# Kernel optimization log

Hardware: AMD Instinct MI355X
Metric: run time of the kernel (lower is better)

The kernel has to match this reference:

```python
import jax, jax.numpy as jnp
import numpy as np

TOP_K = 2
NORM_TOPK = True


def setup_inputs() -> dict:
    key = jax.random.key(0)
    k1, k2, k3, k4 = jax.random.split(key, 4)
    B, S, H = 2, 1024, 2048
    E, I = 16, 768
    hidden_states = jax.random.normal(k1, (B, S, H), dtype=jnp.float32)
    gate_w = jax.random.normal(k2, (E, H), dtype=jnp.float32) * 0.02
    gate_up_w = jax.random.normal(k3, (E, 2 * I, H), dtype=jnp.float32) * 0.02
    down_w = jax.random.normal(k4, (E, H, I), dtype=jnp.float32) * 0.02
    return {
        "hidden_states": hidden_states,
        "gate_w": gate_w,
        "gate_up_w": gate_up_w,
        "down_w": down_w,
        "top_k": TOP_K,
    }


def reference(hidden_states, gate_w, gate_up_w, down_w, top_k):
    B, S, H = hidden_states.shape
    E = gate_w.shape[0]
    x = hidden_states.reshape(-1, H)  # [T, H]
    T = x.shape[0]

    # Router: softmax in float32 (as in torch F.softmax(..., dtype=torch.float))
    router_logits = x @ gate_w.T  # [T, E]
    probs = jax.nn.softmax(router_logits.astype(jnp.float32), axis=-1)
    top_w, top_idx = jax.lax.top_k(probs, top_k)  # [T, k]
    if NORM_TOPK:
        top_w = top_w / jnp.sum(top_w, axis=-1, keepdims=True)
    top_w = top_w.astype(x.dtype)

    # Dense combine weights [T, E]: routing weight where selected, 0 elsewhere.
    comb = jnp.sum(jax.nn.one_hot(top_idx, E, dtype=x.dtype) * top_w[..., None], axis=1)

    # SwiGLU expert MLPs evaluated for all experts, combined with sparse weights.
    gu = jnp.einsum("th,efh->tef", x, gate_up_w)  # [T, E, 2I]
    g, u = jnp.split(gu, 2, axis=-1)
    h = jax.nn.silu(g) * u  # [T, E, I]
    y = jnp.einsum("tei,ehi->teh", h, down_w)  # [T, E, H]
    out = jnp.einsum("teh,te->th", y, comb)  # [T, H]

    return out.reshape(B, S, H), router_logits
```

## Files before the change

### kernel.cpp

```cpp
#include <hip/hip_runtime.h>
#include <hip/hip_bf16.h>
#include <stdint.h>

#define T_TOK 2048
#define H_DIM 2048
#define E_NUM 16
#define I_DIM 768

typedef __bf16 bf16;
typedef __bf16 bf16x4 __attribute__((ext_vector_type(4)));
typedef __bf16 bf16x8 __attribute__((ext_vector_type(8)));
typedef float f32x4 __attribute__((ext_vector_type(4)));

__device__ __forceinline__ void async_cp16(void* l, const void* g) {
    __builtin_amdgcn_global_load_lds(
        (const __attribute__((address_space(1))) void*)g,
        (__attribute__((address_space(3))) void*)l, 16, 0, 0);
}

__global__ __launch_bounds__(256) void router_kernel(
    const float* __restrict__ x, const float* __restrict__ gw,
    float* __restrict__ logits, int* __restrict__ cnt,
    int* __restrict__ tok_list, float* __restrict__ wgt_list,
    bf16* __restrict__ xb)
{
    const int t = blockIdx.x;
    const int tid = threadIdx.x;
    const int lane = tid & 63, wid = tid >> 6;

    double part[E_NUM];
#pragma unroll
    for (int e = 0; e < E_NUM; ++e) part[e] = 0.0;

#pragma unroll
    for (int it = 0; it < 2; ++it) {
        int h = it * 1024 + tid * 4;
        float4 xv = *(const float4*)(x + (size_t)t * H_DIM + h);
        bf16x4 xb4 = { (bf16)xv.x, (bf16)xv.y, (bf16)xv.z, (bf16)xv.w };
        *(bf16x4*)(xb + (size_t)t * H_DIM + h) = xb4;
#pragma unroll
        for (int e = 0; e < E_NUM; ++e) {
            float4 wv = *(const float4*)(gw + (size_t)e * H_DIM + h);
            part[e] += (double)xv.x * (double)wv.x + (double)xv.y * (double)wv.y
                     + (double)xv.z * (double)wv.z + (double)xv.w * (double)wv.w;
        }
    }
#pragma unroll
    for (int off = 32; off > 0; off >>= 1)
#pragma unroll
        for (int e = 0; e < E_NUM; ++e)
            part[e] += __shfl_down(part[e], off);

    __shared__ double sh[4][E_NUM];
    __shared__ float lg[E_NUM];
    if (lane == 0)
#pragma unroll
        for (int e = 0; e < E_NUM; ++e) sh[wid][e] = part[e];
    __syncthreads();
    if (tid < E_NUM) {
        float v = (float)(sh[0][tid] + sh[1][tid] + sh[2][tid] + sh[3][tid]);
        lg[tid] = v;
        logits[(size_t)t * E_NUM + tid] = v;
    }
    __syncthreads();
    if (tid == 0) {
        int i0 = 0; float v0 = lg[0];
#pragma unroll
        for (int e = 1; e < E_NUM; ++e) if (lg[e] > v0) { v0 = lg[e]; i0 = e; }
        int i1 = -1; float v1 = -3.4e38f;
#pragma unroll
        for (int e = 0; e < E_NUM; ++e) if (e != i0 && lg[e] > v1) { v1 = lg[e]; i1 = e; }
        float w0 = 1.0f / (1.0f + __expf(v1 - v0));
        float w1 = 1.0f - w0;
        int p0 = atomicAdd(&cnt[i0], 1);
        tok_list[i0 * T_TOK + p0] = t; wgt_list[i0 * T_TOK + p0] = w0;
        int p1 = atomicAdd(&cnt[i1], 1);
        tok_list[i1 * T_TOK + p1] = t; wgt_list[i1 * T_TOK + p1] = w1;
    }
}

__global__ void scan_kernel(const int* __restrict__ cnt, int* __restrict__ offs)
{
    if (threadIdx.x == 0) {
        int o = 0;
        for (int e = 0; e < E_NUM; ++e) { offs[e] = o; o += cnt[e]; }
    }
}

__global__ __launch_bounds__(256, 2) void gateup_kernel(
    const bf16* __restrict__ xb, const float* __restrict__ gup,
    const int* __restrict__ cnt, const int* __restrict__ offs,
    const int* __restrict__ tok_list, bf16* __restrict__ hbuf)
{
    const int e = blockIdx.z;
    const int count = cnt[e];
    const int row0 = blockIdx.y * 64;
    if (row0 >= count) return;
    const int i0 = blockIdx.x * 64;
    const int hoff = offs[e];
    const int tid = threadIdx.x;
    const int lane = tid & 63, wid = tid >> 6;

    __shared__ __align__(16) bf16 As[2][64 * 64];
    __shared__ __align__(16) float Bs[2][128 * 64];

    int raA0 = tid >> 3, sA0 = tid & 7;
    int raA1 = raA0 + 32;
    int cA0 = sA0 ^ (raA0 & 7);
    int cA1 = sA0 ^ (raA1 & 7);
    int tr0 = row0 + raA0; if (tr0 >= count) tr0 = count - 1;
    int tr1 = row0 + raA1; if (tr1 >= count) tr1 = count - 1;
    const bf16* srcA0 = xb + (size_t)tok_list[e * T_TOK + tr0] * H_DIM + cA0 * 8;
    const bf16* srcA1 = xb + (size_t)tok_list[e * T_TOK + tr1] * H_DIM + cA1 * 8;
    const int dA0 = (wid * 64) * 8;
    const int dA1 = (wid * 64 + 256) * 8;

    const float* srcB[8]; int dB[8];
#pragma unroll
    for (int i = 0; i < 8; ++i) {
        int idx = i * 256 + tid;
        int r = idx >> 4, s = idx & 15;
        int c = s ^ (r & 15);
        int is_u = (r >> 5) & 1;
        int ioff = (r >> 6) * 32 + (r & 31);
        size_t grow = (size_t)e * (2 * I_DIM) + (size_t)is_u * I_DIM + i0 + ioff;
        srcB[i] = gup + grow * H_DIM + c * 4;
        dB[i] = (i * 256 + wid * 64) * 4;
    }

    f32x4 acc[2][4];
#pragma unroll
    for (int a = 0; a < 2; ++a)
#pragma unroll
        for (int b = 0; b < 4; ++b) acc[a][b] = (f32x4){0.f, 0.f, 0.f, 0.f};

    const int la = lane & 15, lq = lane >> 4;
    const int wm = wid >> 1, wn = wid & 1;

    auto stage = [&](int buf, int k0) {
        async_cp16(&As[buf][dA0], srcA0 + k0);
        async_cp16(&As[buf][dA1], srcA1 + k0);
#pragma unroll
        for (int i = 0; i < 8; ++i) async_cp16(&Bs[buf][dB[i]], srcB[i] + k0);
    };

    stage(0, 0);
    __syncthreads();
    int cur = 0;
    for (int k0 = 0; k0 < H_DIM; k0 += 64) {
        if (k0 + 64 < H_DIM) stage(cur ^ 1, k0 + 64);
        const bf16* Asc = As[cur];
        const float* Bsc = Bs[cur];
#pragma unroll
        for (int ks = 0; ks < 2; ++ks) {
            bf16x8 af[2], bfr[4];
            int chA = ks * 4 + lq;
            int c0 = ks * 8 + lq * 2;
#pragma unroll
            for (int mt = 0; mt < 2; ++mt) {
                int row = 32 * wm + 16 * mt + la;
                int sl = chA ^ (row & 7);
                af[mt] = *(const bf16x8*)(Asc + (size_t)(row * 8 + sl) * 8);
            }
#pragma unroll
            for (int nt = 0; nt < 4; ++nt) {
                int row = 64 * wn + 16 * nt + la;
                int s0 = c0 ^ (row & 15);
                int s1 = s0 ^ 1;
                f32x4 v0 = *(const f32x4*)(Bsc + (size_t)(row * 16 + s0) * 4);
                f32x4 v1 = *(const f32x4*)(Bsc + (size_t)(row * 16 + s1) * 4);
                bfr[nt] = (bf16x8){ (bf16)v0.x, (bf16)v0.y, (bf16)v0.z, (bf16)v0.w,
                                    (bf16)v1.x, (bf16)v1.y, (bf16)v1.z, (bf16)v1.w };
            }
#pragma unroll
            for (int mt = 0; mt < 2; ++mt)
#pragma unroll
                for (int nt = 0; nt < 4; ++nt)
                    acc[mt][nt] = __builtin_amdgcn_mfma_f32_16x16x32_bf16(af[mt], bfr[nt], acc[mt][nt], 0, 0, 0);
        }
        __syncthreads();
        cur ^= 1;
    }

#pragma unroll
    for (int mt = 0; mt < 2; ++mt)
#pragma unroll
        for (int p = 0; p < 2; ++p)
#pragma unroll
            for (int r = 0; r < 4; ++r) {
                int trow = 32 * wm + 16 * mt + lq * 4 + r;
                if (row0 + trow < count) {
                    float g = acc[mt][p][r], u = acc[mt][p + 2][r];
                    float hv = (g / (1.0f + __expf(-g))) * u;
                    int col = i0 + 32 * wn + 16 * p + la;
                    hbuf[(size_t)(hoff + row0 + trow) * I_DIM + col] = (bf16)hv;
                }
            }
}

__global__ __launch_bounds__(256, 2) void down_kernel(
    const float* __restrict__ dw, const bf16* __restrict__ hbuf,
    const int* __restrict__ cnt, const int* __restrict__ offs,
    const int* __restrict__ tok_list, const float* __restrict__ wgt_list,
    float* __restrict__ out)
{
    const int e = blockIdx.z;
    const int count = cnt[e];
    const int row0 = blockIdx.y * 64;
    if (row0 >= count) return;
    const int n0 = blockIdx.x * 128;
    const int hoff = offs[e];
    const int tid = threadIdx.x;
    const int lane = tid & 63, wid = tid >> 6;

    __shared__ __align__(16) bf16 As[2][64 * 64];
    __shared__ __align__(16) float Bs[2][128 * 64];

    int raA0 = tid >> 3, sA0 = tid & 7;
    int raA1 = raA0 + 32;
    int cA0 = sA0 ^ (raA0 & 7);
    int cA1 = sA0 ^ (raA1 & 7);
    int ar0 = row0 + raA0; if (ar0 >= count) ar0 = count - 1;
    int ar1 = row0 + raA1; if (ar1 >= count) ar1 = count - 1;
    const bf16* srcA0 = hbuf + (size_t)(hoff + ar0) * I_DIM + cA0 * 8;
    const bf16* srcA1 = hbuf + (size_t)(hoff + ar1) * I_DIM + cA1 * 8;
    const int dA0 = (wid * 64) * 8;
    const int dA1 = (wid * 64 + 256) * 8;

    const float* srcB[8]; int dB[8];
#pragma unroll
    for (int i = 0; i < 8; ++i) {
        int idx = i * 256 + tid;
        int r = idx >> 4, s = idx & 15;
        int c = s ^ (r & 15);
        srcB[i] = dw + ((size_t)e * H_DIM + n0 + r) * I_DIM + c * 4;
        dB[i] = (i * 256 + wid * 64) * 4;
    }

    f32x4 acc[2][4];
#pragma unroll
    for (int a = 0; a < 2; ++a)
#pragma unroll
        for (int b = 0; b < 4; ++b) acc[a][b] = (f32x4){0.f, 0.f, 0.f, 0.f};

    const int la = lane & 15, lq = lane >> 4;
    const int wm = wid >> 1, wn = wid & 1;

    auto stage = [&](int buf, int k0) {
        async_cp16(&As[buf][dA0], srcA0 + k0);
        async_cp16(&As[buf][dA1], srcA1 + k0);
#pragma unroll
        for (int i = 0; i < 8; ++i) async_cp16(&Bs[buf][dB[i]], srcB[i] + k0);
    };

    stage(0, 0);
    __syncthreads();
    int cur = 0;
    for (int k0 = 0; k0 < I_DIM; k0 += 64) {
        if (k0 + 64 < I_DIM) stage(cur ^ 1, k0 + 64);
        const bf16* Asc = As[cur];
        const float* Bsc = Bs[cur];
#pragma unroll
        for (int ks = 0; ks < 2; ++ks) {
            bf16x8 af[2], bfr[4];
            int chA = ks * 4 + lq;
            int c0 = ks * 8 + lq * 2;
#pragma unroll
            for (int mt = 0; mt < 2; ++mt) {
                int row = 32 * wm + 16 * mt + la;
                int sl = chA ^ (row & 7);
                af[mt] = *(const bf16x8*)(Asc + (size_t)(row * 8 + sl) * 8);
            }
#pragma unroll
            for (int nt = 0; nt < 4; ++nt) {
                int row = 64 * wn + 16 * nt + la;
                int s0 = c0 ^ (row & 15);
                int s1 = s0 ^ 1;
                f32x4 v0 = *(const f32x4*)(Bsc + (size_t)(row * 16 + s0) * 4);
                f32x4 v1 = *(const f32x4*)(Bsc + (size_t)(row * 16 + s1) * 4);
                bfr[nt] = (bf16x8){ (bf16)v0.x, (bf16)v0.y, (bf16)v0.z, (bf16)v0.w,
                                    (bf16)v1.x, (bf16)v1.y, (bf16)v1.z, (bf16)v1.w };
            }
#pragma unroll
            for (int mt = 0; mt < 2; ++mt)
#pragma unroll
                for (int nt = 0; nt < 4; ++nt)
                    acc[mt][nt] = __builtin_amdgcn_mfma_f32_16x16x32_bf16(af[mt], bfr[nt], acc[mt][nt], 0, 0, 0);
        }
        __syncthreads();
        cur ^= 1;
    }

#pragma unroll
    for (int mt = 0; mt < 2; ++mt)
#pragma unroll
        for (int nt = 0; nt < 4; ++nt)
#pragma unroll
            for (int r = 0; r < 4; ++r) {
                int trow = 32 * wm + 16 * mt + lq * 4 + r;
                if (row0 + trow < count) {
                    int col = n0 + 64 * wn + 16 * nt + la;
                    int grow = row0 + trow;
                    atomicAdd(&out[(size_t)tok_list[e * T_TOK + grow] * H_DIM + col],
                              wgt_list[e * T_TOK + grow] * acc[mt][nt][r]);
                }
            }
}

extern "C" void kernel_launch(void* const* d_in, const int* in_sizes, int n_in,
                              void* d_out, int out_size, void* d_ws, size_t ws_size,
                              hipStream_t stream)
{
    const float* x   = (const float*)d_in[0];
    const float* gw  = (const float*)d_in[1];
    const float* gup = (const float*)d_in[2];
    const float* dw  = (const float*)d_in[3];
    float* out = (float*)d_out;
    float* logits = out + (size_t)T_TOK * H_DIM;

    char* ws = (char*)d_ws;
    int*   cnt      = (int*)(ws + 0);
    int*   offs     = (int*)(ws + 256);
    int*   tok_list = (int*)(ws + 512);
    float* wgt_list = (float*)(ws + 131584);
    bf16*  hbuf     = (bf16*)(ws + 262656);
    bf16*  xb       = (bf16*)(ws + 6554112);

    hipMemsetAsync(cnt, 0, 256, stream);
    hipMemsetAsync(out, 0, (size_t)T_TOK * H_DIM * sizeof(float), stream);

    router_kernel<<<T_TOK, 256, 0, stream>>>(x, gw, logits, cnt, tok_list, wgt_list, xb);
    scan_kernel<<<1, 64, 0, stream>>>(cnt, offs);
    gateup_kernel<<<dim3(I_DIM / 64, T_TOK / 64, E_NUM), 256, 0, stream>>>(
        xb, gup, cnt, offs, tok_list, hbuf);
    down_kernel<<<dim3(H_DIM / 128, T_TOK / 64, E_NUM), 256, 0, stream>>>(
        dw, hbuf, cnt, offs, tok_list, wgt_list, out);
}
```

Before: 545.7 us.

## Stage fp32 weights through registers and store bf16 tiles in LDS

Both expert GEMM kernels now load the fp32 weight tile into registers, convert it to bf16 once, and write it to shared memory. This replaces async fp32 global-to-LDS copies that were converted on every fragment read. Halving the B tile's shared memory is meant to allow three blocks per CU and cheaper LDS reads. The cost is that the global weight loads now go through registers, so latency hiding depends on overlapping them with the MFMA work, and register pressure rises.

```diff
diff --git a/kernel.cpp b/kernel.cpp
--- a/kernel.cpp
+++ b/kernel.cpp
@@ -87,7 +87,7 @@
     }
 }
 
-__global__ __launch_bounds__(256, 2) void gateup_kernel(
+__global__ __launch_bounds__(256, 3) void gateup_kernel(
     const bf16* __restrict__ xb, const float* __restrict__ gup,
     const int* __restrict__ cnt, const int* __restrict__ offs,
     const int* __restrict__ tok_list, bf16* __restrict__ hbuf)
@@ -102,7 +102,7 @@
     const int lane = tid & 63, wid = tid >> 6;
 
     __shared__ __align__(16) bf16 As[2][64 * 64];
-    __shared__ __align__(16) float Bs[2][128 * 64];
+    __shared__ __align__(16) bf16 Bs[2][128 * 64];
 
     int raA0 = tid >> 3, sA0 = tid & 7;
     int raA1 = raA0 + 32;
@@ -115,17 +115,17 @@
     const int dA0 = (wid * 64) * 8;
     const int dA1 = (wid * 64 + 256) * 8;
 
-    const float* srcB[8]; int dB[8];
-#pragma unroll
-    for (int i = 0; i < 8; ++i) {
+    const float* srcB[4]; int dB[4];
+#pragma unroll
+    for (int i = 0; i < 4; ++i) {
         int idx = i * 256 + tid;
-        int r = idx >> 4, s = idx & 15;
-        int c = s ^ (r & 15);
+        int r = idx >> 3, s = idx & 7;
+        int gc = s ^ (r & 7);
         int is_u = (r >> 5) & 1;
         int ioff = (r >> 6) * 32 + (r & 31);
         size_t grow = (size_t)e * (2 * I_DIM) + (size_t)is_u * I_DIM + i0 + ioff;
-        srcB[i] = gup + grow * H_DIM + c * 4;
-        dB[i] = (i * 256 + wid * 64) * 4;
+        srcB[i] = gup + grow * H_DIM + gc * 8;
+        dB[i] = (r * 8 + s) * 8;
     }
 
     f32x4 acc[2][4];
@@ -137,40 +137,54 @@
     const int la = lane & 15, lq = lane >> 4;
     const int wm = wid >> 1, wn = wid & 1;
 
-    auto stage = [&](int buf, int k0) {
-        async_cp16(&As[buf][dA0], srcA0 + k0);
-        async_cp16(&As[buf][dA1], srcA1 + k0);
-#pragma unroll
-        for (int i = 0; i < 8; ++i) async_cp16(&Bs[buf][dB[i]], srcB[i] + k0);
-    };
-
-    stage(0, 0);
+    f32x4 bv[4][2];
+    auto loadB = [&](int k0) {
+#pragma unroll
+        for (int i = 0; i < 4; ++i) {
+            bv[i][0] = *(const f32x4*)(srcB[i] + k0);
+            bv[i][1] = *(const f32x4*)(srcB[i] + k0 + 4);
+        }
+    };
+    auto storeB = [&](bf16* B) {
+#pragma unroll
+        for (int i = 0; i < 4; ++i) {
+            bf16x8 w = { (bf16)bv[i][0].x, (bf16)bv[i][0].y, (bf16)bv[i][0].z, (bf16)bv[i][0].w,
+                         (bf16)bv[i][1].x, (bf16)bv[i][1].y, (bf16)bv[i][1].z, (bf16)bv[i][1].w };
+            *(bf16x8*)(B + dB[i]) = w;
+        }
+    };
+    auto loadA = [&](bf16* A, int k0) {
+        async_cp16(A + dA0, srcA0 + k0);
+        async_cp16(A + dA1, srcA1 + k0);
+    };
+
+    loadB(0);
+    loadA(As[0], 0);
+    storeB(Bs[0]);
     __syncthreads();
+
+    const int NK = H_DIM / 64;
     int cur = 0;
-    for (int k0 = 0; k0 < H_DIM; k0 += 64) {
-        if (k0 + 64 < H_DIM) stage(cur ^ 1, k0 + 64);
+    for (int kt = 0; kt < NK; ++kt) {
+        const int nxt = cur ^ 1;
+        const bool pf = (kt + 1 < NK);
+        if (pf) { loadB((kt + 1) * 64); loadA(As[nxt], (kt + 1) * 64); }
         const bf16* Asc = As[cur];
-        const float* Bsc = Bs[cur];
+        const bf16* Bsc = Bs[cur];
 #pragma unroll
         for (int ks = 0; ks < 2; ++ks) {
             bf16x8 af[2], bfr[4];
-            int chA = ks * 4 + lq;
-            int c0 = ks * 8 + lq * 2;
+            const int chA = ks * 4 + lq;
+            const int sl = chA ^ (la & 7);
 #pragma unroll
             for (int mt = 0; mt < 2; ++mt) {
                 int row = 32 * wm + 16 * mt + la;
-                int sl = chA ^ (row & 7);
                 af[mt] = *(const bf16x8*)(Asc + (size_t)(row * 8 + sl) * 8);
             }
 #pragma unroll
             for (int nt = 0; nt < 4; ++nt) {
                 int row = 64 * wn + 16 * nt + la;
-                int s0 = c0 ^ (row & 15);
-                int s1 = s0 ^ 1;
-                f32x4 v0 = *(const f32x4*)(Bsc + (size_t)(row * 16 + s0) * 4);
-                f32x4 v1 = *(const f32x4*)(Bsc + (size_t)(row * 16 + s1) * 4);
-                bfr[nt] = (bf16x8){ (bf16)v0.x, (bf16)v0.y, (bf16)v0.z, (bf16)v0.w,
-                                    (bf16)v1.x, (bf16)v1.y, (bf16)v1.z, (bf16)v1.w };
+                bfr[nt] = *(const bf16x8*)(Bsc + (size_t)(row * 8 + sl) * 8);
             }
 #pragma unroll
             for (int mt = 0; mt < 2; ++mt)
@@ -178,8 +192,9 @@
                 for (int nt = 0; nt < 4; ++nt)
                     acc[mt][nt] = __builtin_amdgcn_mfma_f32_16x16x32_bf16(af[mt], bfr[nt], acc[mt][nt], 0, 0, 0);
         }
+        if (pf) storeB(Bs[nxt]);
         __syncthreads();
-        cur ^= 1;
+        cur = nxt;
     }
 
 #pragma unroll
@@ -198,7 +213,7 @@
             }
 }
 
-__global__ __launch_bounds__(256, 2) void down_kernel(
+__global__ __launch_bounds__(256, 3) void down_kernel(
     const float* __restrict__ dw, const bf16* __restrict__ hbuf,
     const int* __restrict__ cnt, const int* __restrict__ offs,
     const int* __restrict__ tok_list, const float* __restrict__ wgt_list,
@@ -214,7 +229,7 @@
     const int lane = tid & 63, wid = tid >> 6;
 
     __shared__ __align__(16) bf16 As[2][64 * 64];
-    __shared__ __align__(16) float Bs[2][128 * 64];
+    __shared__ __align__(16) bf16 Bs[2][128 * 64];
 
     int raA0 = tid >> 3, sA0 = tid & 7;
     int raA1 = raA0 + 32;
@@ -227,14 +242,14 @@
     const int dA0 = (wid * 64) * 8;
     const int dA1 = (wid * 64 + 256) * 8;
 
-    const float* srcB[8]; int dB[8];
-#pragma unroll
-    for (int i = 0; i < 8; ++i) {
+    const float* srcB[4]; int dB[4];
+#pragma unroll
+    for (int i = 0; i < 4; ++i) {
         int idx = i * 256 + tid;
-        int r = idx >> 4, s = idx & 15;
-        int c = s ^ (r & 15);
-        srcB[i] = dw + ((size_t)e * H_DIM + n0 + r) * I_DIM + c * 4;
-        dB[i] = (i * 256 + wid * 64) * 4;
+        int r = idx >> 3, s = idx & 7;
+        int gc = s ^ (r & 7);
+        srcB[i] = dw + ((size_t)e * H_DIM + n0 + r) * I_DIM + gc * 8;
+        dB[i] = (r * 8 + s) * 8;
     }
 
     f32x4 acc[2][4];
@@ -246,40 +261,54 @@
     const int la = lane & 15, lq = lane >> 4;
     const int wm = wid >> 1, wn = wid & 1;
 
-    auto stage = [&](int buf, int k0) {
-        async_cp16(&As[buf][dA0], srcA0 + k0);
-        async_cp16(&As[buf][dA1], srcA1 + k0);
-#pragma unroll
-        for (int i = 0; i < 8; ++i) async_cp16(&Bs[buf][dB[i]], srcB[i] + k0);
-    };
-
-    stage(0, 0);
+    f32x4 bv[4][2];
+    auto loadB = [&](int k0) {
+#pragma unroll
+        for (int i = 0; i < 4; ++i) {
+            bv[i][0] = *(const f32x4*)(srcB[i] + k0);
+            bv[i][1] = *(const f32x4*)(srcB[i] + k0 + 4);
+        }
+    };
+    auto storeB = [&](bf16* B) {
+#pragma unroll
+        for (int i = 0; i < 4; ++i) {
+            bf16x8 w = { (bf16)bv[i][0].x, (bf16)bv[i][0].y, (bf16)bv[i][0].z, (bf16)bv[i][0].w,
+                         (bf16)bv[i][1].x, (bf16)bv[i][1].y, (bf16)bv[i][1].z, (bf16)bv[i][1].w };
+            *(bf16x8*)(B + dB[i]) = w;
+        }
+    };
+    auto loadA = [&](bf16* A, int k0) {
+        async_cp16(A + dA0, srcA0 + k0);
+        async_cp16(A + dA1, srcA1 + k0);
+    };
+
+    loadB(0);
+    loadA(As[0], 0);
+    storeB(Bs[0]);
     __syncthreads();
+
+    const int NK = I_DIM / 64;
     int cur = 0;
-    for (int k0 = 0; k0 < I_DIM; k0 += 64) {
-        if (k0 + 64 < I_DIM) stage(cur ^ 1, k0 + 64);
+    for (int kt = 0; kt < NK; ++kt) {
+        const int nxt = cur ^ 1;
+        const bool pf = (kt + 1 < NK);
+        if (pf) { loadB((kt + 1) * 64); loadA(As[nxt], (kt + 1) * 64); }
         const bf16* Asc = As[cur];
-        const float* Bsc = Bs[cur];
+        const bf16* Bsc = Bs[cur];
 #pragma unroll
         for (int ks = 0; ks < 2; ++ks) {
             bf16x8 af[2], bfr[4];
-            int chA = ks * 4 + lq;
-            int c0 = ks * 8 + lq * 2;
+            const int chA = ks * 4 + lq;
+            const int sl = chA ^ (la & 7);
 #pragma unroll
             for (int mt = 0; mt < 2; ++mt) {
                 int row = 32 * wm + 16 * mt + la;
-                int sl = chA ^ (row & 7);
                 af[mt] = *(const bf16x8*)(Asc + (size_t)(row * 8 + sl) * 8);
             }
 #pragma unroll
             for (int nt = 0; nt < 4; ++nt) {
                 int row = 64 * wn + 16 * nt + la;
-                int s0 = c0 ^ (row & 15);
-                int s1 = s0 ^ 1;
-                f32x4 v0 = *(const f32x4*)(Bsc + (size_t)(row * 16 + s0) * 4);
-                f32x4 v1 = *(const f32x4*)(Bsc + (size_t)(row * 16 + s1) * 4);
-                bfr[nt] = (bf16x8){ (bf16)v0.x, (bf16)v0.y, (bf16)v0.z, (bf16)v0.w,
-                                    (bf16)v1.x, (bf16)v1.y, (bf16)v1.z, (bf16)v1.w };
+                bfr[nt] = *(const bf16x8*)(Bsc + (size_t)(row * 8 + sl) * 8);
             }
 #pragma unroll
             for (int mt = 0; mt < 2; ++mt)
@@ -287,8 +316,9 @@
                 for (int nt = 0; nt < 4; ++nt)
                     acc[mt][nt] = __builtin_amdgcn_mfma_f32_16x16x32_bf16(af[mt], bfr[nt], acc[mt][nt], 0, 0, 0);
         }
+        if (pf) storeB(Bs[nxt]);
         __syncthreads();
-        cur ^= 1;
+        cur = nxt;
     }
 
 #pragma unroll
```

New measurement: 555.0 us. About the same (+1.7%).
